# Kernel tuning notes

Measured on AMD Instinct MI355X. Metric: run time of the kernel, lower is better.

Reference implementation:

```python
import jax, jax.numpy as jnp
import numpy as np

B, S, N, E = 8, 32, 2000, 64000
GH, H = 32, 64  # gat_h, lstm hidden
NEG_SLOPE = 0.2


def setup_inputs() -> dict:
    key = jax.random.key(0)
    ks = jax.random.split(key, 12)
    f32 = jnp.float32
    x = jax.random.normal(ks[0], (B, S, N), f32)
    edge_index = jax.random.randint(ks[1], (2, E), 0, N)
    # GATConv(1, GH, heads=1, concat=False): lin weight [GH,1] -> vector, att_src/att_dst [GH], bias [GH]
    w_lin = jax.random.normal(ks[2], (GH,), f32)
    att_src = jax.random.normal(ks[3], (GH,), f32) * 0.1
    att_dst = jax.random.normal(ks[4], (GH,), f32) * 0.1
    gat_bias = jax.random.normal(ks[5], (GH,), f32) * 0.01
    D = GH * N  # LSTM input size
    W_ih = jax.random.normal(ks[6], (4 * H, D), f32) * (1.0 / np.sqrt(D))
    W_hh = jax.random.normal(ks[7], (4 * H, H), f32) * (1.0 / np.sqrt(H))
    b_ih = jax.random.normal(ks[8], (4 * H,), f32) * 0.01
    b_hh = jax.random.normal(ks[9], (4 * H,), f32) * 0.01
    W_head = jax.random.normal(ks[10], (N, H), f32) * (1.0 / np.sqrt(H))
    b_head = jax.random.normal(ks[11], (N,), f32) * 0.01
    return {"x": x, "edge_index": edge_index, "w_lin": w_lin, "att_src": att_src,
            "att_dst": att_dst, "gat_bias": gat_bias, "W_ih": W_ih, "W_hh": W_hh,
            "b_ih": b_ih, "b_hh": b_hh, "W_head": W_head, "b_head": b_head}


def reference(x, edge_index, w_lin, att_src, att_dst, gat_bias,
              W_ih, W_hh, b_ih, b_hh, W_head, b_head):
    x = x.astype(jnp.float32)
    # --- GAT (in_channels=1, heads=1), batched over (B,S) ---
    # PyG default: add self-loops
    loops = jnp.arange(N)
    ei = jnp.concatenate([edge_index, jnp.stack([loops, loops])], axis=1)
    src, dst = ei[0], ei[1]  # [Et], Et = E + N
    # lifted feature h_n = x_n * w_lin (rank-1), so attention logits are scalar per node
    a_src = x * jnp.dot(w_lin, att_src)  # [B,S,N]
    a_dst = x * jnp.dot(w_lin, att_dst)  # [B,S,N]
    e = jax.nn.leaky_relu(a_src[..., src] + a_dst[..., dst], NEG_SLOPE)  # [B,S,Et]
    e = jnp.moveaxis(e, -1, 0)  # [Et,B,S] (segment axis leading)
    seg_max = jax.ops.segment_max(e, dst, num_segments=N)  # [N,B,S]
    e = jnp.exp(e - seg_max[dst])
    denom = jax.ops.segment_sum(e, dst, num_segments=N)  # [N,B,S]
    alpha = e / denom[dst]  # edge softmax over incoming edges
    x_src = jnp.moveaxis(x[..., src], -1, 0)  # [Et,B,S]
    agg = jax.ops.segment_sum(alpha * x_src, dst, num_segments=N)  # [N,B,S]
    agg = jnp.moveaxis(agg, 0, -1)  # [B,S,N]
    # outer product with w_lin restores [.,GH]; add bias, then relu (from forward)
    h = jax.nn.relu(agg[..., None] * w_lin + gat_bias)  # [B,S,N,GH]
    lstm_in = h.reshape(B, S, N * GH)

    # --- LSTM (1 layer, batch_first), keep final hidden state ---
    def step(carry, xt):
        hp, cp = carry
        gates = xt @ W_ih.T + b_ih + hp @ W_hh.T + b_hh  # [B,4H]
        i, f, g, o = jnp.split(gates, 4, axis=-1)
        c = jax.nn.sigmoid(f) * cp + jax.nn.sigmoid(i) * jnp.tanh(g)
        hn = jax.nn.sigmoid(o) * jnp.tanh(c)
        return (hn, c), None

    h0 = jnp.zeros((B, H), jnp.float32)
    c0 = jnp.zeros((B, H), jnp.float32)
    (hT, _), _ = jax.lax.scan(step, (h0, c0), jnp.swapaxes(lstm_in, 0, 1))
    return hT @ W_head.T + b_head  # [B,N]
```

## Files before the change

kernel.cpp:

```cpp
#include <hip/hip_runtime.h>
#include <hip/hip_bf16.h>
#include <cstddef>
#include <cstdint>

#define B_  8
#define S_  32
#define BT_ 256
#define N_  2000
#define E_  64000
#define GH_ 32
#define H_  64
#define G4_ 256
#define D_  64000
#define NEG_SLOPE_ 0.2f

#define KC_   125
#define NPC_  16

typedef __attribute__((ext_vector_type(8))) short short8;
typedef __attribute__((ext_vector_type(4))) float floatx4;
union U8 { uint32_t u[4]; short8 s; };

__device__ __forceinline__ float fsigmoid(float x) { return 1.0f / (1.0f + __expf(-x)); }
__device__ __forceinline__ float ftanh_(float x)   { return 1.0f - 2.0f / (__expf(2.0f * x) + 1.0f); }

__device__ __forceinline__ void split2(float v0, float v1, uint32_t& hi, uint32_t& lo) {
  uint32_t b0 = __float_as_uint(v0), b1 = __float_as_uint(v1);
  hi = __builtin_amdgcn_perm(b1, b0, 0x07060302u);
  float l0 = v0 - __uint_as_float(b0 & 0xffff0000u);
  float l1 = v1 - __uint_as_float(b1 & 0xffff0000u);
  lo = __builtin_amdgcn_perm(__float_as_uint(l1), __float_as_uint(l0), 0x07060302u);
}


__global__ __launch_bounds__(256) void hist_kernel(
    const int* __restrict__ ei, int* __restrict__ deg)
{
  const int i = blockIdx.x * 256 + threadIdx.x;
  if (i < E_) atomicAdd(&deg[ei[E_ + i]], 1);
}

__global__ __launch_bounds__(256) void scan_kernel(
    const int* __restrict__ deg, int* __restrict__ rowptr, int* __restrict__ cursor)
{
  __shared__ int tsum[256];
  const int tid = threadIdx.x;
  int v[8];
  int s = 0;
  const int base = tid * 8;
#pragma unroll
  for (int j = 0; j < 8; ++j) {
    const int idx = base + j;
    const int d = (idx < N_) ? deg[idx] : 0;
    v[j] = s;
    s += d;
  }
  tsum[tid] = s;
  __syncthreads();
  for (int off = 1; off < 256; off <<= 1) {
    int t = 0;
    if (tid >= off) t = tsum[tid - off];
    __syncthreads();
    tsum[tid] += t;
    __syncthreads();
  }
  const int ebase = tsum[tid] - s;
#pragma unroll
  for (int j = 0; j < 8; ++j) {
    const int idx = base + j;
    if (idx < N_) {
      const int r = ebase + v[j];
      rowptr[idx] = r;
      cursor[idx] = r;
    }
  }
  if (tid == 0) rowptr[N_] = E_;
}

__global__ __launch_bounds__(256) void scatter_kernel(
    const int* __restrict__ ei, int* __restrict__ cursor, int* __restrict__ csr_src)
{
  const int i = blockIdx.x * 256 + threadIdx.x;
  if (i >= E_) return;
  const int s = ei[i];
  const int d = ei[E_ + i];
  const int pos = atomicAdd(&cursor[d], 1);
  csr_src[pos] = s;
}

__global__ __launch_bounds__(256) void transpose_kernel(
    const float* __restrict__ x, float* __restrict__ xT)
{
  __shared__ float tile[32][33];
  const int tx = threadIdx.x & 31;
  const int ty = threadIdx.x >> 5;
  const int n0  = blockIdx.x * 32;
  const int bt0 = blockIdx.y * 32;
#pragma unroll
  for (int r = 0; r < 4; ++r) {
    const int bt = bt0 + ty + r * 8;
    const int nn = n0 + tx;
    if (nn < N_) tile[ty + r * 8][tx] = x[(size_t)bt * N_ + nn];
  }
  __syncthreads();
#pragma unroll
  for (int r = 0; r < 4; ++r) {
    const int n = n0 + ty + r * 8;
    if (n < N_) xT[(size_t)n * BT_ + bt0 + tx] = tile[tx][ty + r * 8];
  }
}

__global__ __launch_bounds__(256) void gat_gather_kernel(
    const float* __restrict__ xT, const int* __restrict__ rowptr,
    const int* __restrict__ csr_src,
    const float* __restrict__ w_lin, const float* __restrict__ att_src,
    const float* __restrict__ att_dst, float* __restrict__ agg_T)
{
  __shared__ int srcs[512];
  const int n   = blockIdx.x;
  const int tid = threadIdx.x;

  float c_s = 0.f, c_d = 0.f;
#pragma unroll
  for (int g = 0; g < GH_; ++g) {
    const float w = w_lin[g];
    c_s += w * att_src[g];
    c_d += w * att_dst[g];
  }

  const int r0 = rowptr[n];
  const int r1 = rowptr[n + 1];
  const int d  = r1 - r0;

  const float xn = xT[(size_t)n * BT_ + tid];
  const float ad = c_d * xn;
  float e = (c_s + c_d) * xn;
  e = e > 0.f ? e : NEG_SLOPE_ * e;
  float w = __expf(e);
  float num = w * xn;
  float den = w;

  for (int base = 0; base < d; base += 512) {
    const int cnt = min(512, d - base);
    __syncthreads();
    for (int i = tid; i < cnt; i += 256) srcs[i] = csr_src[r0 + base + i];
    __syncthreads();

    int p = 0;
    for (; p + 4 <= cnt; p += 4) {
      const int s0 = srcs[p], s1 = srcs[p + 1], s2 = srcs[p + 2], s3 = srcs[p + 3];
      const float x0 = xT[(size_t)s0 * BT_ + tid];
      const float x1 = xT[(size_t)s1 * BT_ + tid];
      const float x2 = xT[(size_t)s2 * BT_ + tid];
      const float x3 = xT[(size_t)s3 * BT_ + tid];
      float e0 = fmaf(c_s, x0, ad); e0 = e0 > 0.f ? e0 : NEG_SLOPE_ * e0;
      float e1 = fmaf(c_s, x1, ad); e1 = e1 > 0.f ? e1 : NEG_SLOPE_ * e1;
      float e2 = fmaf(c_s, x2, ad); e2 = e2 > 0.f ? e2 : NEG_SLOPE_ * e2;
      float e3 = fmaf(c_s, x3, ad); e3 = e3 > 0.f ? e3 : NEG_SLOPE_ * e3;
      const float w0 = __expf(e0), w1 = __expf(e1), w2 = __expf(e2), w3 = __expf(e3);
      num = fmaf(w0, x0, num); den += w0;
      num = fmaf(w1, x1, num); den += w1;
      num = fmaf(w2, x2, num); den += w2;
      num = fmaf(w3, x3, num); den += w3;
    }
    for (; p < cnt; ++p) {
      const int s = srcs[p];
      const float xs = xT[(size_t)s * BT_ + tid];
      float ee = fmaf(c_s, xs, ad);
      ee = ee > 0.f ? ee : NEG_SLOPE_ * ee;
      const float ww = __expf(ee);
      num = fmaf(ww, xs, num);
      den += ww;
    }
  }
  agg_T[(size_t)n * BT_ + tid] = num / den;
}

__global__ __launch_bounds__(256) void gate_mfma_kernel(
    const float* __restrict__ W_ih, const float* __restrict__ agg_T,
    const float* __restrict__ w_lin, const float* __restrict__ gat_bias,
    float* __restrict__ partial, float* __restrict__ pre_gates, int use_atomic)
{
  __shared__ float agg_s[NPC_ * 256];

  const int tid  = threadIdx.x;
  const int nb   = blockIdx.x;
  const int kc   = blockIdx.y;
  const int n0   = kc * NPC_;
  const int wv   = tid >> 6;
  const int lane = tid & 63;
  const int i16  = lane & 15;
  const int q    = lane >> 4;
  const int j0   = nb * 64;

  {
    const float4* src = (const float4*)(agg_T + (size_t)n0 * 256);
    float4* dst = (float4*)agg_s;
#pragma unroll
    for (int p = 0; p < 4; ++p) dst[tid + p * 256] = src[tid + p * 256];
  }

  float wlr[8], gbr[8];
#pragma unroll
  for (int jx = 0; jx < 8; ++jx) {
    wlr[jx] = w_lin[q * 8 + jx];
    gbr[jx] = gat_bias[q * 8 + jx];
  }

  floatx4 acc[4][4];
#pragma unroll
  for (int mt = 0; mt < 4; ++mt)
#pragma unroll
    for (int jt = 0; jt < 4; ++jt)
#pragma unroll
      for (int r = 0; r < 4; ++r) acc[mt][jt][r] = 0.f;

  const float* Wr[4];
#pragma unroll
  for (int jt = 0; jt < 4; ++jt)
    Wr[jt] = W_ih + (size_t)(j0 + jt * 16 + i16) * D_ + (size_t)n0 * GH_ + q * 8;

  float4 cb[8];
#pragma unroll
  for (int jt = 0; jt < 4; ++jt) {
    cb[2 * jt]     = *(const float4*)(Wr[jt]);
    cb[2 * jt + 1] = *(const float4*)(Wr[jt] + 4);
  }

  __syncthreads();

#pragma unroll 1
  for (int nn = 0; nn < NPC_; ++nn) {
    const int nnx = (nn + 1) & (NPC_ - 1);

    short8 ah[4], al[4];
#pragma unroll
    for (int mt = 0; mt < 4; ++mt) {
      const float a = agg_s[nn * 256 + wv * 64 + mt * 16 + i16];
      U8 Hh, Ll;
#pragma unroll
      for (int p = 0; p < 4; ++p) {
        float v0 = fmaf(a, wlr[2 * p],     gbr[2 * p]);
        float v1 = fmaf(a, wlr[2 * p + 1], gbr[2 * p + 1]);
        v0 = fmaxf(v0, 0.f);
        v1 = fmaxf(v1, 0.f);
        split2(v0, v1, Hh.u[p], Ll.u[p]);
      }
      ah[mt] = Hh.s; al[mt] = Ll.s;
    }

#pragma unroll
    for (int jt = 0; jt < 4; ++jt) {
      short8 bh, bl;
      {
        U8 Hh, Ll;
        split2(cb[2 * jt].x,     cb[2 * jt].y,     Hh.u[0], Ll.u[0]);
        split2(cb[2 * jt].z,     cb[2 * jt].w,     Hh.u[1], Ll.u[1]);
        split2(cb[2 * jt + 1].x, cb[2 * jt + 1].y, Hh.u[2], Ll.u[2]);
        split2(cb[2 * jt + 1].z, cb[2 * jt + 1].w, Hh.u[3], Ll.u[3]);
        bh = Hh.s; bl = Ll.s;
      }
      cb[2 * jt]     = *(const float4*)(Wr[jt] + nnx * GH_);
      cb[2 * jt + 1] = *(const float4*)(Wr[jt] + nnx * GH_ + 4);
#pragma unroll
      for (int mt = 0; mt < 4; ++mt) {
        acc[mt][jt] = __builtin_amdgcn_mfma_f32_16x16x32_bf16(ah[mt], bh, acc[mt][jt], 0, 0, 0);
        acc[mt][jt] = __builtin_amdgcn_mfma_f32_16x16x32_bf16(al[mt], bh, acc[mt][jt], 0, 0, 0);
        acc[mt][jt] = __builtin_amdgcn_mfma_f32_16x16x32_bf16(ah[mt], bl, acc[mt][jt], 0, 0, 0);
      }
    }
  }

#pragma unroll
  for (int mt = 0; mt < 4; ++mt) {
    const int bt = wv * 64 + mt * 16 + q * 4;
#pragma unroll
    for (int jt = 0; jt < 4; ++jt) {
      const int j = j0 + jt * 16 + i16;
      if (use_atomic) {
#pragma unroll
        for (int r = 0; r < 4; ++r) atomicAdd(&pre_gates[(bt + r) * G4_ + j], acc[mt][jt][r]);
      } else {
#pragma unroll
        for (int r = 0; r < 4; ++r)
          partial[((size_t)kc * 256 + (bt + r)) * 256 + j] = acc[mt][jt][r];
      }
    }
  }
}

__global__ __launch_bounds__(256) void reduce_kernel(
    const float* __restrict__ partial, float* __restrict__ pre_gates)
{
  const int o = blockIdx.x * 256 + threadIdx.x;
  float s0 = 0.f, s1 = 0.f, s2 = 0.f, s3 = 0.f;
  int kc = 0;
  for (; kc + 4 <= KC_; kc += 4) {
    s0 += partial[(size_t)(kc + 0) * 65536 + o];
    s1 += partial[(size_t)(kc + 1) * 65536 + o];
    s2 += partial[(size_t)(kc + 2) * 65536 + o];
    s3 += partial[(size_t)(kc + 3) * 65536 + o];
  }
  for (; kc < KC_; ++kc) s0 += partial[(size_t)kc * 65536 + o];
  pre_gates[o] = (s0 + s1) + (s2 + s3);
}

__global__ __launch_bounds__(256) void lstm_kernel(
    const float* __restrict__ pre_gates, const float* __restrict__ W_hh,
    const float* __restrict__ b_ih, const float* __restrict__ b_hh,
    float* __restrict__ hT)
{
  const int b   = blockIdx.x;
  const int tid = threadIdx.x;
  __shared__ float h_s[H_];
  __shared__ float g_s[G4_];

  float wr[H_];
#pragma unroll
  for (int k = 0; k < H_; ++k) wr[k] = W_hh[(size_t)tid * H_ + k];

  float pg[S_];
#pragma unroll
  for (int t = 0; t < S_; ++t) pg[t] = pre_gates[(size_t)(b * S_ + t) * G4_ + tid];

  const float bias = b_ih[tid] + b_hh[tid];
  if (tid < H_) h_s[tid] = 0.f;
  float c = 0.f;
  __syncthreads();

  for (int t = 0; t < S_; ++t) {
    float g0 = pg[t] + bias, g1 = 0.f, g2 = 0.f, g3 = 0.f;
#pragma unroll
    for (int k = 0; k < H_; k += 4) {
      g0 = fmaf(wr[k + 0], h_s[k + 0], g0);
      g1 = fmaf(wr[k + 1], h_s[k + 1], g1);
      g2 = fmaf(wr[k + 2], h_s[k + 2], g2);
      g3 = fmaf(wr[k + 3], h_s[k + 3], g3);
    }
    g_s[tid] = (g0 + g1) + (g2 + g3);
    __syncthreads();
    if (tid < H_) {
      const float ig = fsigmoid(g_s[tid]);
      const float fg = fsigmoid(g_s[H_ + tid]);
      const float gg = ftanh_(g_s[2 * H_ + tid]);
      const float og = fsigmoid(g_s[3 * H_ + tid]);
      c = fg * c + ig * gg;
      h_s[tid] = og * ftanh_(c);
    }
    __syncthreads();
  }
  if (tid < H_) hT[b * H_ + tid] = h_s[tid];
}

__global__ __launch_bounds__(256) void head_kernel(
    const float* __restrict__ hT, const float* __restrict__ W_head,
    const float* __restrict__ b_head, float* __restrict__ out)
{
  const int o = blockIdx.x * 256 + threadIdx.x;
  if (o >= B_ * N_) return;
  const int b = o / N_;
  const int n = o - b * N_;
  const float4* w4 = (const float4*)(W_head + (size_t)n * H_);
  const float4* h4 = (const float4*)(hT + (size_t)b * H_);
  float acc = b_head[n];
#pragma unroll
  for (int q = 0; q < H_ / 4; ++q) {
    const float4 w = w4[q];
    const float4 h = h4[q];
    acc += w.x * h.x + w.y * h.y + w.z * h.z + w.w * h.w;
  }
  out[o] = acc;
}

extern "C" void kernel_launch(void* const* d_in, const int* in_sizes, int n_in,
                              void* d_out, int out_size, void* d_ws, size_t ws_size,
                              hipStream_t stream) {
  const float* x        = (const float*)d_in[0];
  const int*   ei       = (const int*)  d_in[1];
  const float* w_lin    = (const float*)d_in[2];
  const float* att_src  = (const float*)d_in[3];
  const float* att_dst  = (const float*)d_in[4];
  const float* gat_bias = (const float*)d_in[5];
  const float* W_ih     = (const float*)d_in[6];
  const float* W_hh     = (const float*)d_in[7];
  const float* b_ih     = (const float*)d_in[8];
  const float* b_hh     = (const float*)d_in[9];
  const float* W_head   = (const float*)d_in[10];
  const float* b_head   = (const float*)d_in[11];
  float* out = (float*)d_out;

  char* ws = (char*)d_ws;
  float* agg_T     = (float*)(ws + 0);
  float* pre_gates = (float*)(ws + 2048000);
  float* hT        = (float*)(ws + 2310144);
  float* xT        = (float*)(ws + 2312192);
  int*   deg       = (int*)  (ws + 4360192);
  int*   rowptr    = (int*)  (ws + 4368384);
  int*   cursor    = (int*)  (ws + 4376576);
  int*   csr_src   = (int*)  (ws + 4384768);
  float* partial   = (float*)(ws + 4640768);
  const size_t need = 4640768 + (size_t)KC_ * 65536 * sizeof(float);
  const int use_atomic = (ws_size < need) ? 1 : 0;

  hipMemsetAsync(deg, 0, N_ * sizeof(int), stream);
  hist_kernel<<<dim3((E_ + 255) / 256), dim3(256), 0, stream>>>(ei, deg);
  scan_kernel<<<dim3(1), dim3(256), 0, stream>>>(deg, rowptr, cursor);
  scatter_kernel<<<dim3((E_ + 255) / 256), dim3(256), 0, stream>>>(ei, cursor, csr_src);
  transpose_kernel<<<dim3((N_ + 31) / 32, BT_ / 32), dim3(256), 0, stream>>>(x, xT);
  gat_gather_kernel<<<dim3(N_), dim3(256), 0, stream>>>(
      xT, rowptr, csr_src, w_lin, att_src, att_dst, agg_T);

  if (use_atomic) {
    hipMemsetAsync(pre_gates, 0, G4_ * BT_ * sizeof(float), stream);
  }
  gate_mfma_kernel<<<dim3(4, KC_), dim3(256), 0, stream>>>(
      W_ih, agg_T, w_lin, gat_bias, partial, pre_gates, use_atomic);
  if (!use_atomic) {
    reduce_kernel<<<dim3(256), dim3(256), 0, stream>>>(partial, pre_gates);
  }

  lstm_kernel<<<dim3(B_), dim3(256), 0, stream>>>(pre_gates, W_hh, b_ih, b_hh, hT);
  head_kernel<<<dim3((B_ * N_ + 255) / 256), dim3(256), 0, stream>>>(hT, W_head, b_head, out);
}
```

Measured before the change: 225.6 us.

## Fuse histogram with transpose, unroll gather by 8, split gate GEMM launch

Merges the degree histogram and the x transpose into one 504-block launch to remove a kernel launch. Adds an 8-way unrolled loop in the GAT gather so more independent loads are in flight. Splits the gate MFMA launch into two launches over chunk ranges through a new kc offset parameter. That split adds a launch and has no clear benefit.

```diff
diff --git a/kernel.cpp b/kernel.cpp
--- a/kernel.cpp
+++ b/kernel.cpp
@@ -16,6 +16,7 @@
 
 #define KC_   125
 #define NPC_  16
+#define KCA_  63
 
 typedef __attribute__((ext_vector_type(8))) short short8;
 typedef __attribute__((ext_vector_type(4))) float floatx4;
@@ -33,11 +34,34 @@
 }
 
 
-__global__ __launch_bounds__(256) void hist_kernel(
-    const int* __restrict__ ei, int* __restrict__ deg)
-{
-  const int i = blockIdx.x * 256 + threadIdx.x;
-  if (i < E_) atomicAdd(&deg[ei[E_ + i]], 1);
+__global__ __launch_bounds__(256) void hist_transpose_kernel(
+    const int* __restrict__ ei, int* __restrict__ deg,
+    const float* __restrict__ x, float* __restrict__ xT)
+{
+  const int bid = blockIdx.x;
+  const int tid = threadIdx.x;
+
+  if (bid < (E_ + 255) / 256) {
+    const int i = bid * 256 + tid;
+    if (i < E_) atomicAdd(&deg[ei[E_ + i]], 1);
+  }
+
+  __shared__ float tile[32][33];
+  const int tx = tid & 31;
+  const int ty = tid >> 5;
+  const int bx = bid % 63, by = bid / 63;
+  const int n0 = bx * 32, bt0 = by * 32;
+#pragma unroll
+  for (int r = 0; r < 4; ++r) {
+    const int nn = n0 + tx;
+    if (nn < N_) tile[ty + r * 8][tx] = x[(size_t)(bt0 + ty + r * 8) * N_ + nn];
+  }
+  __syncthreads();
+#pragma unroll
+  for (int r = 0; r < 4; ++r) {
+    const int n = n0 + ty + r * 8;
+    if (n < N_) xT[(size_t)n * BT_ + bt0 + tx] = tile[tx][ty + r * 8];
+  }
 }
 
 __global__ __launch_bounds__(256) void scan_kernel(
@@ -86,28 +110,6 @@
   const int d = ei[E_ + i];
   const int pos = atomicAdd(&cursor[d], 1);
   csr_src[pos] = s;
-}
-
-__global__ __launch_bounds__(256) void transpose_kernel(
-    const float* __restrict__ x, float* __restrict__ xT)
-{
-  __shared__ float tile[32][33];
-  const int tx = threadIdx.x & 31;
-  const int ty = threadIdx.x >> 5;
-  const int n0  = blockIdx.x * 32;
-  const int bt0 = blockIdx.y * 32;
-#pragma unroll
-  for (int r = 0; r < 4; ++r) {
-    const int bt = bt0 + ty + r * 8;
-    const int nn = n0 + tx;
-    if (nn < N_) tile[ty + r * 8][tx] = x[(size_t)bt * N_ + nn];
-  }
-  __syncthreads();
-#pragma unroll
-  for (int r = 0; r < 4; ++r) {
-    const int n = n0 + ty + r * 8;
-    if (n < N_) xT[(size_t)n * BT_ + bt0 + tx] = tile[tx][ty + r * 8];
-  }
 }
 
 __global__ __launch_bounds__(256) void gat_gather_kernel(
@@ -147,6 +149,22 @@
     __syncthreads();
 
     int p = 0;
+    for (; p + 8 <= cnt; p += 8) {
+      int   si[8];
+      float xi[8];
+#pragma unroll
+      for (int u = 0; u < 8; ++u) si[u] = srcs[p + u];
+#pragma unroll
+      for (int u = 0; u < 8; ++u) xi[u] = xT[(size_t)si[u] * BT_ + tid];
+#pragma unroll
+      for (int u = 0; u < 8; ++u) {
+        float ee = fmaf(c_s, xi[u], ad);
+        ee = ee > 0.f ? ee : NEG_SLOPE_ * ee;
+        const float ww = __expf(ee);
+        num = fmaf(ww, xi[u], num);
+        den += ww;
+      }
+    }
     for (; p + 4 <= cnt; p += 4) {
       const int s0 = srcs[p], s1 = srcs[p + 1], s2 = srcs[p + 2], s3 = srcs[p + 3];
       const float x0 = xT[(size_t)s0 * BT_ + tid];
@@ -179,13 +197,14 @@
 __global__ __launch_bounds__(256) void gate_mfma_kernel(
     const float* __restrict__ W_ih, const float* __restrict__ agg_T,
     const float* __restrict__ w_lin, const float* __restrict__ gat_bias,
-    float* __restrict__ partial, float* __restrict__ pre_gates, int use_atomic)
+    float* __restrict__ partial, float* __restrict__ pre_gates,
+    int use_atomic, int kc_ofs)
 {
   __shared__ float agg_s[NPC_ * 256];
 
   const int tid  = threadIdx.x;
   const int nb   = blockIdx.x;
-  const int kc   = blockIdx.y;
+  const int kc   = blockIdx.y + kc_ofs;
   const int n0   = kc * NPC_;
   const int wv   = tid >> 6;
   const int lane = tid & 63;
@@ -403,18 +422,19 @@
   const int use_atomic = (ws_size < need) ? 1 : 0;
 
   hipMemsetAsync(deg, 0, N_ * sizeof(int), stream);
-  hist_kernel<<<dim3((E_ + 255) / 256), dim3(256), 0, stream>>>(ei, deg);
+  hist_transpose_kernel<<<dim3(504), dim3(256), 0, stream>>>(ei, deg, x, xT);
   scan_kernel<<<dim3(1), dim3(256), 0, stream>>>(deg, rowptr, cursor);
   scatter_kernel<<<dim3((E_ + 255) / 256), dim3(256), 0, stream>>>(ei, cursor, csr_src);
-  transpose_kernel<<<dim3((N_ + 31) / 32, BT_ / 32), dim3(256), 0, stream>>>(x, xT);
   gat_gather_kernel<<<dim3(N_), dim3(256), 0, stream>>>(
       xT, rowptr, csr_src, w_lin, att_src, att_dst, agg_T);
 
   if (use_atomic) {
     hipMemsetAsync(pre_gates, 0, G4_ * BT_ * sizeof(float), stream);
   }
-  gate_mfma_kernel<<<dim3(4, KC_), dim3(256), 0, stream>>>(
-      W_ih, agg_T, w_lin, gat_bias, partial, pre_gates, use_atomic);
+  gate_mfma_kernel<<<dim3(4, KCA_), dim3(256), 0, stream>>>(
+      W_ih, agg_T, w_lin, gat_bias, partial, pre_gates, use_atomic, 0);
+  gate_mfma_kernel<<<dim3(4, KC_ - KCA_), dim3(256), 0, stream>>>(
+      W_ih, agg_T, w_lin, gat_bias, partial, pre_gates, use_atomic, KCA_);
   if (!use_atomic) {
     reduce_kernel<<<dim3(256), dim3(256), 0, stream>>>(partial, pre_gates);
   }
```

Result: slower. 231.3 us (+2.5%).
